# Optimization experiments

Measured on AMD Instinct MI355X. Metric: run time of the kernel, lower is better.

The kernel has to match this reference:

```python
import jax, jax.numpy as jnp
import numpy as np

N = 32768          # nodes
E = 131072         # edges
H = 4              # heads
RNA = 128          # rna_feature_dim
PROT = 32          # prot_feature_dim
F0 = 64            # num_features_per_layer[0] == [1]
CIN = F0 + PROT    # cross-path feature dim (96)
LRELU = 0.2


def _param(key, shape):
    return jax.random.normal(key, shape, dtype=jnp.float32) * 0.1


def setup_inputs() -> dict:
    key = jax.random.key(0)
    ks = jax.random.split(key, 20)
    return {
        "rna_data": jax.random.normal(ks[0], (N, RNA), dtype=jnp.float32),
        "prot_data": jax.random.normal(ks[1], (N, PROT), dtype=jnp.float32),
        "edge_index": jax.random.randint(ks[2], (2, E), 0, N, dtype=jnp.int32),
        "W_gat_proj": _param(ks[3], (RNA, F0)),
        "b_gat_proj": _param(ks[4], (F0,)),
        "W_gat_reproj": _param(ks[5], (F0, RNA)),
        "b_gat_reproj": _param(ks[6], (RNA,)),
        "Wg": _param(ks[7], (F0, H * F0)),
        "ag_src": _param(ks[8], (H, F0)),
        "ag_trg": _param(ks[9], (H, F0)),
        "bg": _param(ks[10], (F0,)),
        "W_cross_proj": _param(ks[11], (RNA + PROT, CIN)),
        "b_cross_proj": _param(ks[12], (CIN,)),
        "W_cross_reproj": _param(ks[13], (CIN, RNA + PROT)),
        "b_cross_reproj": _param(ks[14], (RNA + PROT,)),
        "Wc": _param(ks[15], (CIN, H * CIN)),
        "ac_src": _param(ks[16], (H, CIN)),
        "ac_trg": _param(ks[17], (H, CIN)),
        "bc": _param(ks[18], (CIN,)),
    }


def gat_layer(x, W, a_src, a_trg, bias, edge_index, softmax_on_src):
    """GATLayer with concat=False, activation=None, skip connection (in==out dim),
    dropout in eval mode. CrossAttnLayer groups the edge-softmax by src instead of trg."""
    n, f = x.shape
    src, trg = edge_index[0], edge_index[1]
    proj = (x @ W).reshape(n, H, f)                               # [N,H,F] lift targets
    s_src = jnp.einsum('nhf,hf->nh', proj, a_src)                 # [N,H]
    s_trg = jnp.einsum('nhf,hf->nh', proj, a_trg)                 # [N,H]
    scores = jax.nn.leaky_relu(s_src[src] + s_trg[trg], LRELU)    # [E,H] per-edge scores
    grp = src if softmax_on_src else trg
    ex = jnp.exp(scores - scores.max())                           # global-max shift (as in source)
    denom = jax.ops.segment_sum(ex, grp, num_segments=n)          # [N,H]
    attn = ex / (denom[grp] + 1e-16)                              # neighborhood-aware softmax [E,H]
    weighted = proj[src] * attn[:, :, None]                       # [E,H,F]
    out = jax.ops.segment_sum(weighted, trg, num_segments=n)      # scatter-add aggregate [N,H,F]
    out = out + x[:, None, :]                                     # direct skip (out_dim == in_dim)
    out = out.mean(axis=1) + bias                                 # concat=False -> head mean, + bias
    return out                                                    # activation=None (last layer)


def reference(rna_data, prot_data, edge_index,
              W_gat_proj, b_gat_proj, W_gat_reproj, b_gat_reproj,
              Wg, ag_src, ag_trg, bg,
              W_cross_proj, b_cross_proj, W_cross_reproj, b_cross_reproj,
              Wc, ac_src, ac_trg, bc):
    concat = jnp.concatenate([rna_data, prot_data], axis=1)       # [N, RNA+PROT]
    rna_p = rna_data @ W_gat_proj + b_gat_proj                    # [N, F0]
    cross_p = concat @ W_cross_proj + b_cross_proj                # [N, CIN]
    gat_out = gat_layer(rna_p, Wg, ag_src, ag_trg, bg, edge_index, False)    # [N, F0]
    cross_out = gat_layer(cross_p, Wc, ac_src, ac_trg, bc, edge_index, True)  # [N, CIN]
    # CrossAttnLayer's trailing view(-1, num_heads, num_out_features)
    cross_out = cross_out.reshape(-1, H, CIN)                     # [N/H, H, CIN]
    gat_final = gat_out @ W_gat_reproj + b_gat_reproj             # [N, RNA]
    cross_final = cross_out @ W_cross_reproj + b_cross_reproj     # [N/H, H, RNA+PROT]
    return gat_final, cross_final
```

## Files before the change

kernel.cpp:

```cpp
#include <hip/hip_runtime.h>
#include <hip/hip_bf16.h>

#define NN 32768
#define NE 131072
#define HH 4

constexpr float kLrelu = 0.2f;

using bf16x8 = __attribute__((ext_vector_type(8))) __bf16;
using f32x4  = __attribute__((ext_vector_type(4))) float;

__device__ inline short f2b(float f) {
    __hip_bfloat16 h = __float2bfloat16(f);
    return __builtin_bit_cast(short, h);
}
__device__ inline float b2f(short s) {
    __hip_bfloat16 h = __builtin_bit_cast(__hip_bfloat16, s);
    return __bfloat162float(h);
}
__device__ inline float blo(int u) {
    return __builtin_bit_cast(float, (int)(u << 16));
}
__device__ inline float bhi(int u) {
    return __builtin_bit_cast(float, (int)(u & 0xffff0000));
}
__device__ inline float lrexp(float x) {
    return __expf(x > 0.f ? x : kLrelu * x);
}

template<int K, int LDA, int OUTN, int BM, int BN, bool BF16OUT>
__global__ __launch_bounds__(256) void mfma_gemm(
    const short* __restrict__ A, const short* __restrict__ Wt,
    const float* __restrict__ bias,
    float* __restrict__ Cf, short* __restrict__ Cb)
{
    constexpr int KP    = K + 8;
    constexpr int WM    = BM / 32;
    constexpr int WN    = 4 / WM;
    constexpr int WBN   = BN / WN;
    constexpr int CF    = WBN / 16;
    constexpr int CPR   = K / 8;
    constexpr int TOT   = (BM + BN) * KP;
    constexpr int SLICE = TOT / 4;

    __shared__ short lds[TOT];
    short* As = lds;
    short* Bs = lds + BM * KP;

    const int tid  = threadIdx.x;
    const int wave = tid >> 6;
    const int lane = tid & 63;
    const int lr   = lane & 15;
    const int kb   = lane >> 4;
    const int wm   = wave % WM;
    const int wn   = wave / WM;
    const int row0 = blockIdx.x * BM;
    const int col0 = blockIdx.y * BN;

    #pragma unroll
    for (int g = tid; g < BM * CPR; g += 256) {
        int r = g / CPR, c = g - r * CPR;
        bf16x8 v = *(const bf16x8*)(A + (size_t)(row0 + r) * LDA + c * 8);
        *(bf16x8*)(As + r * KP + c * 8) = v;
    }
    #pragma unroll
    for (int g = tid; g < BN * CPR; g += 256) {
        int r = g / CPR, c = g - r * CPR;
        bf16x8 v = *(const bf16x8*)(Wt + (size_t)(col0 + r) * K + c * 8);
        *(bf16x8*)(Bs + r * KP + c * 8) = v;
    }
    __syncthreads();

    f32x4 acc[2][CF] = {};
    #pragma unroll
    for (int k0 = 0; k0 < K; k0 += 32) {
        bf16x8 af0 = *(const bf16x8*)(As + (wm * 32 + lr     ) * KP + k0 + kb * 8);
        bf16x8 af1 = *(const bf16x8*)(As + (wm * 32 + lr + 16) * KP + k0 + kb * 8);
        #pragma unroll
        for (int cf = 0; cf < CF; ++cf) {
            bf16x8 bv = *(const bf16x8*)(Bs + (wn * WBN + cf * 16 + lr) * KP + k0 + kb * 8);
            acc[0][cf] = __builtin_amdgcn_mfma_f32_16x16x32_bf16(af0, bv, acc[0][cf], 0, 0, 0);
            acc[1][cf] = __builtin_amdgcn_mfma_f32_16x16x32_bf16(af1, bv, acc[1][cf], 0, 0, 0);
        }
    }

    #pragma unroll
    for (int mf = 0; mf < 2; ++mf) {
        __syncthreads();
        if constexpr (BF16OUT) {
            constexpr int LEP = WBN + 8;
            short* ep = lds + wave * SLICE;
            #pragma unroll
            for (int cf = 0; cf < CF; ++cf) {
                const int c  = cf * 16 + lr;
                const float bv = bias ? bias[col0 + wn * WBN + c] : 0.0f;
                #pragma unroll
                for (int j = 0; j < 4; ++j)
                    ep[(kb * 4 + j) * LEP + c] = f2b(acc[mf][cf][j] + bv);
            }
            __syncthreads();
            constexpr int CROW = WBN / 8;
            for (int g = lane; g < 16 * CROW; g += 64) {
                int r = g / CROW, cc = g - r * CROW;
                bf16x8 v = *(const bf16x8*)(ep + r * LEP + cc * 8);
                *(bf16x8*)(Cb + (size_t)(row0 + wm * 32 + mf * 16 + r) * OUTN
                              + col0 + wn * WBN + cc * 8) = v;
            }
        } else {
            constexpr int LEPF = WBN + 4;
            float* epf = (float*)(lds + wave * SLICE);
            #pragma unroll
            for (int cf = 0; cf < CF; ++cf) {
                const int c  = cf * 16 + lr;
                const float bv = bias ? bias[col0 + wn * WBN + c] : 0.0f;
                #pragma unroll
                for (int j = 0; j < 4; ++j)
                    epf[(kb * 4 + j) * LEPF + c] = acc[mf][cf][j] + bv;
            }
            __syncthreads();
            constexpr int CROWF = WBN / 4;
            for (int g = lane; g < 16 * CROWF; g += 64) {
                int r = g / CROWF, cc = g - r * CROWF;
                float4 v = *(const float4*)(epf + r * LEPF + cc * 4);
                *(float4*)(Cf + (size_t)(row0 + wm * 32 + mf * 16 + r) * OUTN
                              + col0 + wn * WBN + cc * 4) = v;
            }
        }
    }
}

template<int F>
__device__ inline void score_one(
    const short* __restrict__ proj_b,
    const float* __restrict__ a_src, const float* __restrict__ a_trg,
    float* __restrict__ ssrc, float* __restrict__ strg, int t)
{
    int n = t >> 2, h = t & 3;
    const int4* p = (const int4*)(proj_b + (size_t)n * (4 * F) + h * F);
    const float* as = a_src + h * F;
    const float* at = a_trg + h * F;
    float ss = 0.f, st = 0.f;
    #pragma unroll
    for (int c = 0; c < F / 8; ++c) {
        int4 v = p[c];
        int u[4] = { v.x, v.y, v.z, v.w };
        #pragma unroll
        for (int q = 0; q < 4; ++q) {
            float x0 = blo(u[q]), x1 = bhi(u[q]);
            ss += x0 * as[c * 8 + 2 * q] + x1 * as[c * 8 + 2 * q + 1];
            st += x0 * at[c * 8 + 2 * q] + x1 * at[c * 8 + 2 * q + 1];
        }
    }
    ssrc[t] = ss;
    strg[t] = st;
}

__global__ __launch_bounds__(256) void scores_both(
    const short* __restrict__ projG,
    const float* __restrict__ agsG, const float* __restrict__ agtG,
    float* __restrict__ ssrcG, float* __restrict__ strgG,
    const short* __restrict__ projC,
    const float* __restrict__ acsC, const float* __restrict__ actC,
    float* __restrict__ ssrcC, float* __restrict__ strgC)
{
    int t = blockIdx.x * 256 + threadIdx.x;
    if (t < NN * HH) score_one<64>(projG, agsG, agtG, ssrcG, strgG, t);
    else             score_one<96>(projC, acsC, actC, ssrcC, strgC, t - NN * HH);
}

__global__ __launch_bounds__(256) void prep_kernel(
    const float* __restrict__ rna, const float* __restrict__ prot,
    short* __restrict__ cb,
    const float* W0, const float* W1, const float* W2,
    const float* W3, const float* W4, const float* W5,
    short* T0, short* T1, short* T2, short* T3, short* T4, short* T5,
    int4* __restrict__ zero_p)
{
    const int bid = blockIdx.x;
    if (bid < 5120) {
        int t = bid * 256 + threadIdx.x;
        int n = t / 40, j = (t - n * 40) * 4;
        float4 v = (j < 128) ? *(const float4*)(rna  + (size_t)n * 128 + j)
                             : *(const float4*)(prot + (size_t)n * 32 + (j - 128));
        short4 o = { f2b(v.x), f2b(v.y), f2b(v.z), f2b(v.w) };
        *(short4*)(cb + (size_t)n * 160 + j) = o;
    } else if (bid < 5984) {
        int idx = bid - 5120;
        int wsel = idx / 144, sub = idx - wsel * 144;
        int K, N; const float* W; short* T;
        switch (wsel) {
            case 0: K = 128; N =  64; W = W0; T = T0; break;
            case 1: K =  64; N = 256; W = W1; T = T1; break;
            case 2: K =  64; N = 128; W = W2; T = T2; break;
            case 3: K = 160; N =  96; W = W3; T = T3; break;
            case 4: K =  96; N = 384; W = W4; T = T4; break;
            default:K =  96; N = 160; W = W5; T = T5; break;
        }
        int t = sub * 256 + threadIdx.x;
        if (t >= K * N) return;
        int n = t / K, k = t - n * K;
        T[t] = f2b(W[(size_t)k * N + n]);
    } else {
        zero_p[(bid - 5984) * 256 + threadIdx.x] = make_int4(0, 0, 0, 0);
    }
}

__global__ __launch_bounds__(256) void hist_dual(const int* __restrict__ ei,
                                                 int* __restrict__ deg_t,
                                                 int* __restrict__ deg_s)
{
    int e = blockIdx.x * 256 + threadIdx.x;
    if (e >= NE) return;
    atomicAdd(&deg_s[ei[e]], 1);
    atomicAdd(&deg_t[ei[NE + e]], 1);
}

__global__ __launch_bounds__(1024) void scan_dual(
    const int* __restrict__ deg_t, int* __restrict__ rowptr_t, int* __restrict__ cursor_t,
    const int* __restrict__ deg_s, int* __restrict__ rowptr_s, int* __restrict__ cursor_s)
{
    const int* deg    = blockIdx.x ? deg_s    : deg_t;
    int*       rowptr = blockIdx.x ? rowptr_s : rowptr_t;
    int*       cursor = blockIdx.x ? cursor_s : cursor_t;
    __shared__ int sums[1024];
    const int t = threadIdx.x;
    const int base = t * 32;
    int local[32];
    int s = 0;
    #pragma unroll
    for (int i = 0; i < 32; ++i) { local[i] = s; s += deg[base + i]; }
    sums[t] = s;
    __syncthreads();
    for (int off = 1; off < 1024; off <<= 1) {
        int v = (t >= off) ? sums[t - off] : 0;
        __syncthreads();
        sums[t] += v;
        __syncthreads();
    }
    const int prev = (t == 0) ? 0 : sums[t - 1];
    #pragma unroll
    for (int i = 0; i < 32; ++i) {
        rowptr[base + i] = prev + local[i];
        cursor[base + i] = prev + local[i];
    }
    if (t == 1023) rowptr[NN] = prev + s;
}

__global__ __launch_bounds__(256) void scatter_dual(
    const int* __restrict__ ei,
    int* __restrict__ cursor_t, int* __restrict__ csr_srcT,
    int* __restrict__ cursor_s, int* __restrict__ csr_trgS)
{
    int e = blockIdx.x * 256 + threadIdx.x;
    if (e >= NE) return;
    int s = ei[e], t = ei[NE + e];
    int st = atomicAdd(&cursor_t[t], 1);
    csr_srcT[st] = s;
    int ss = atomicAdd(&cursor_s[s], 1);
    csr_trgS[ss] = t;
}

__global__ __launch_bounds__(256) void den_src_kernel(
    const int* __restrict__ rowptr_s, const int* __restrict__ csr_trgS,
    const float* __restrict__ ssrc, const float* __restrict__ strg,
    float* __restrict__ recip)
{
    int n = blockIdx.x * 256 + threadIdx.x;
    if (n >= NN) return;
    const int beg = rowptr_s[n], end = rowptr_s[n + 1];
    const float4 sv = *(const float4*)(ssrc + 4 * (size_t)n);
    float d0 = 0.f, d1 = 0.f, d2 = 0.f, d3 = 0.f;
    for (int sl = beg; sl < end; ++sl) {
        const int t = csr_trgS[sl];
        const float4 tv = *(const float4*)(strg + 4 * (size_t)t);
        d0 += lrexp(sv.x + tv.x); d1 += lrexp(sv.y + tv.y);
        d2 += lrexp(sv.z + tv.z); d3 += lrexp(sv.w + tv.w);
    }
    *(float4*)(recip + 4 * (size_t)n) =
        make_float4(1.f / (d0 + 1e-16f), 1.f / (d1 + 1e-16f),
                    1.f / (d2 + 1e-16f), 1.f / (d3 + 1e-16f));
}

template<int F, int NPB, bool GROUP_SRC>
__global__ __launch_bounds__((F / 2) * NPB) void aggregate_fused(
    const int* __restrict__ rowptr_t, const int* __restrict__ csr_srcT,
    const float* __restrict__ ssrc, const float* __restrict__ strg,
    const float* __restrict__ recip,
    const short* __restrict__ proj_b,
    const short* __restrict__ x_pb, const float* __restrict__ bias,
    short* __restrict__ aggb)
{
    const int f2   = threadIdx.x * 2;
    const int node = blockIdx.x * NPB + threadIdx.y;
    const int beg  = rowptr_t[node], end = rowptr_t[node + 1];
    const float4 stv = *(const float4*)(strg + 4 * (size_t)node);

    float a0 = 0.f, a1 = 0.f;
    float h0l = 0.f, h1l = 0.f, h2l = 0.f, h3l = 0.f;
    float h0h = 0.f, h1h = 0.f, h2h = 0.f, h3h = 0.f;
    float d0 = 0.f, d1 = 0.f, d2 = 0.f, d3 = 0.f;

    #pragma unroll 4
    for (int sl = beg; sl < end; ++sl) {
        const int s = csr_srcT[sl];
        const float4 sv = *(const float4*)(ssrc + 4 * (size_t)s);
        float e0 = lrexp(sv.x + stv.x);
        float e1 = lrexp(sv.y + stv.y);
        float e2 = lrexp(sv.z + stv.z);
        float e3 = lrexp(sv.w + stv.w);
        const short* p = proj_b + (size_t)s * (4 * F) + f2;
        const int u0 = *(const int*)(p);
        const int u1 = *(const int*)(p + F);
        const int u2 = *(const int*)(p + 2 * F);
        const int u3 = *(const int*)(p + 3 * F);
        if constexpr (GROUP_SRC) {
            const float4 rc = *(const float4*)(recip + 4 * (size_t)s);
            e0 *= rc.x; e1 *= rc.y; e2 *= rc.z; e3 *= rc.w;
            a0 += e0 * blo(u0) + e1 * blo(u1) + e2 * blo(u2) + e3 * blo(u3);
            a1 += e0 * bhi(u0) + e1 * bhi(u1) + e2 * bhi(u2) + e3 * bhi(u3);
        } else {
            d0 += e0; d1 += e1; d2 += e2; d3 += e3;
            h0l += e0 * blo(u0); h0h += e0 * bhi(u0);
            h1l += e1 * blo(u1); h1h += e1 * bhi(u1);
            h2l += e2 * blo(u2); h2h += e2 * bhi(u2);
            h3l += e3 * blo(u3); h3h += e3 * bhi(u3);
        }
    }
    if constexpr (!GROUP_SRC) {
        const float r0 = 1.f / (d0 + 1e-16f), r1 = 1.f / (d1 + 1e-16f);
        const float r2 = 1.f / (d2 + 1e-16f), r3 = 1.f / (d3 + 1e-16f);
        a0 = h0l * r0 + h1l * r1 + h2l * r2 + h3l * r3;
        a1 = h0h * r0 + h1h * r1 + h2h * r2 + h3h * r3;
    }
    const int o = node * F + f2;
    const int ux = *(const int*)(x_pb + o);
    const float v0 = a0 * 0.25f + blo(ux) + bias[f2];
    const float v1 = a1 * 0.25f + bhi(ux) + bias[f2 + 1];
    *(int*)(aggb + o) = (f2b(v0) & 0xffff) | ((int)f2b(v1) << 16);
}

extern "C" void kernel_launch(void* const* d_in, const int* in_sizes, int n_in,
                              void* d_out, int out_size, void* d_ws, size_t ws_size,
                              hipStream_t stream)
{
    const float* rna   = (const float*)d_in[0];
    const float* prot  = (const float*)d_in[1];
    const int*   ei    = (const int*)  d_in[2];
    const float* Wgp   = (const float*)d_in[3];
    const float* bgp   = (const float*)d_in[4];
    const float* Wgr   = (const float*)d_in[5];
    const float* bgr   = (const float*)d_in[6];
    const float* Wg    = (const float*)d_in[7];
    const float* ags   = (const float*)d_in[8];
    const float* agt   = (const float*)d_in[9];
    const float* bg    = (const float*)d_in[10];
    const float* Wcp   = (const float*)d_in[11];
    const float* bcp   = (const float*)d_in[12];
    const float* Wcr   = (const float*)d_in[13];
    const float* bcr   = (const float*)d_in[14];
    const float* Wc    = (const float*)d_in[15];
    const float* acs   = (const float*)d_in[16];
    const float* act   = (const float*)d_in[17];
    const float* bc    = (const float*)d_in[18];

    float* out_gat   = (float*)d_out;
    float* out_cross = out_gat + (size_t)NN * 128;

    float* ssrcG  = (float*)d_ws;
    float* strgG  = ssrcG + (size_t)NN * 4;
    float* ssrcC  = strgG + (size_t)NN * 4;
    float* strgC  = ssrcC + (size_t)NN * 4;
    float* recip  = strgC + (size_t)NN * 4;
    short* projG  = (short*)(recip + (size_t)NN * 4);
    short* projC  = projG + (size_t)NN * 256;
    short* cb     = projC + (size_t)NN * 384;
    short* x_pG   = cb    + (size_t)NN * 160;
    short* x_pC   = x_pG  + (size_t)NN * 64;
    short* aggG   = x_pC  + (size_t)NN * 96;
    short* aggC   = aggG  + (size_t)NN * 64;
    short* wt_gp  = aggC  + (size_t)NN * 96;
    short* wt_g   = wt_gp + 128 * 64;
    short* wt_gr  = wt_g  + 64 * 256;
    short* wt_cp  = wt_gr + 64 * 128;
    short* wt_c   = wt_cp + 160 * 96;
    short* wt_cr  = wt_c  + 96 * 384;
    int*   deg_t  = (int*)(wt_cr + 96 * 160);
    int*   deg_s  = deg_t  + NN;
    int*   cursor_t = deg_s  + NN;
    int*   cursor_s = cursor_t + NN;
    int*   rowptr_t = cursor_s + NN;
    int*   rowptr_s = rowptr_t + NN + 1;
    int*   csr_srcT = rowptr_s + NN + 1;
    int*   csr_trgS = csr_srcT + NE;

    prep_kernel<<<6048, 256, 0, stream>>>(rna, prot, cb,
                                          Wgp, Wg, Wgr, Wcp, Wc, Wcr,
                                          wt_gp, wt_g, wt_gr, wt_cp, wt_c, wt_cr,
                                          (int4*)deg_t);
    hist_dual<<<NE / 256, 256, 0, stream>>>(ei, deg_t, deg_s);
    scan_dual<<<2, 1024, 0, stream>>>(deg_t, rowptr_t, cursor_t, deg_s, rowptr_s, cursor_s);
    scatter_dual<<<NE / 256, 256, 0, stream>>>(ei, cursor_t, csr_srcT, cursor_s, csr_trgS);

    mfma_gemm<128, 160,  64, 32,  64, true ><<<dim3(1024, 1), 256, 0, stream>>>(cb,   wt_gp, bgp, nullptr, x_pG);
    mfma_gemm<160, 160,  96, 64,  96, true ><<<dim3( 512, 1), 256, 0, stream>>>(cb,   wt_cp, bcp, nullptr, x_pC);
    mfma_gemm< 64,  64, 256, 64, 128, true ><<<dim3( 512, 2), 256, 0, stream>>>(x_pG, wt_g,  nullptr, nullptr, projG);
    mfma_gemm< 96,  96, 384, 64, 128, true ><<<dim3( 512, 3), 256, 0, stream>>>(x_pC, wt_c,  nullptr, nullptr, projC);

    scores_both<<<(2 * NN * HH) / 256, 256, 0, stream>>>(
        projG, ags, agt, ssrcG, strgG, projC, acs, act, ssrcC, strgC);
    den_src_kernel<<<NN / 256, 256, 0, stream>>>(rowptr_s, csr_trgS, ssrcC, strgC, recip);

    aggregate_fused<64, 8, false><<<NN / 8, dim3(32, 8), 0, stream>>>(
        rowptr_t, csr_srcT, ssrcG, strgG, nullptr, projG, x_pG, bg, aggG);
    aggregate_fused<96, 8, true><<<NN / 8, dim3(48, 8), 0, stream>>>(
        rowptr_t, csr_srcT, ssrcC, strgC, recip, projC, x_pC, bc, aggC);

    mfma_gemm< 64,  64, 128, 64,  64, false><<<dim3(512, 2), 256, 0, stream>>>(aggG, wt_gr, bgr, out_gat, nullptr);
    mfma_gemm< 96,  96, 160, 64, 160, false><<<dim3(512, 1), 256, 0, stream>>>(aggC, wt_cr, bcr, out_cross, nullptr);
}
```

Measured before the change: 182.0 us.

## Merge paired GEMM and aggregation launches into combined dual-grid kernels

```diff
diff --git a/kernel.cpp b/kernel.cpp
--- a/kernel.cpp
+++ b/kernel.cpp
@@ -29,10 +29,11 @@
 }
 
 template<int K, int LDA, int OUTN, int BM, int BN, bool BF16OUT>
-__global__ __launch_bounds__(256) void mfma_gemm(
+__device__ __forceinline__ void gemm_dev(
     const short* __restrict__ A, const short* __restrict__ Wt,
     const float* __restrict__ bias,
-    float* __restrict__ Cf, short* __restrict__ Cb)
+    float* __restrict__ Cf, short* __restrict__ Cb,
+    short* lds, int bx, int by)
 {
     constexpr int KP    = K + 8;
     constexpr int WM    = BM / 32;
@@ -43,7 +44,6 @@
     constexpr int TOT   = (BM + BN) * KP;
     constexpr int SLICE = TOT / 4;
 
-    __shared__ short lds[TOT];
     short* As = lds;
     short* Bs = lds + BM * KP;
 
@@ -54,8 +54,8 @@
     const int kb   = lane >> 4;
     const int wm   = wave % WM;
     const int wn   = wave / WM;
-    const int row0 = blockIdx.x * BM;
-    const int col0 = blockIdx.y * BN;
+    const int row0 = bx * BM;
+    const int col0 = by * BN;
 
     #pragma unroll
     for (int g = tid; g < BM * CPR; g += 256) {
@@ -129,6 +129,29 @@
     }
 }
 
+template<int K1, int LDA1, int OUTN1, int BM1, int BN1, bool BO1,
+         int K2, int LDA2, int OUTN2, int BM2, int BN2, bool BO2>
+__global__ __launch_bounds__(256) void dual_gemm(
+    const short* A1, const short* Wt1, const float* b1, float* Cf1, short* Cb1,
+    int nbx1, int nby1,
+    const short* A2, const short* Wt2, const float* b2, float* Cf2, short* Cb2,
+    int nbx2, int nby2)
+{
+    constexpr int TOT1 = (BM1 + BN1) * (K1 + 8);
+    constexpr int TOT2 = (BM2 + BN2) * (K2 + 8);
+    constexpr int TOT  = TOT1 > TOT2 ? TOT1 : TOT2;
+    __shared__ short lds[TOT];
+    if (blockIdx.z == 0) {
+        if ((int)blockIdx.x < nbx1 && (int)blockIdx.y < nby1)
+            gemm_dev<K1, LDA1, OUTN1, BM1, BN1, BO1>(A1, Wt1, b1, Cf1, Cb1, lds,
+                                                     blockIdx.x, blockIdx.y);
+    } else {
+        if ((int)blockIdx.x < nbx2 && (int)blockIdx.y < nby2)
+            gemm_dev<K2, LDA2, OUTN2, BM2, BN2, BO2>(A2, Wt2, b2, Cf2, Cb2, lds,
+                                                     blockIdx.x, blockIdx.y);
+    }
+}
+
 template<int F>
 __device__ inline void score_one(
     const short* __restrict__ proj_b,
@@ -281,8 +304,9 @@
                     1.f / (d2 + 1e-16f), 1.f / (d3 + 1e-16f));
 }
 
-template<int F, int NPB, bool GROUP_SRC>
-__global__ __launch_bounds__((F / 2) * NPB) void aggregate_fused(
+template<int F, bool GROUP_SRC>
+__device__ __forceinline__ void agg_body(
+    int f2, int node,
     const int* __restrict__ rowptr_t, const int* __restrict__ csr_srcT,
     const float* __restrict__ ssrc, const float* __restrict__ strg,
     const float* __restrict__ recip,
@@ -290,9 +314,7 @@
     const short* __restrict__ x_pb, const float* __restrict__ bias,
     short* __restrict__ aggb)
 {
-    const int f2   = threadIdx.x * 2;
-    const int node = blockIdx.x * NPB + threadIdx.y;
-    const int beg  = rowptr_t[node], end = rowptr_t[node + 1];
+    const int beg = rowptr_t[node], end = rowptr_t[node + 1];
     const float4 stv = *(const float4*)(strg + 4 * (size_t)node);
 
     float a0 = 0.f, a1 = 0.f;
@@ -300,7 +322,7 @@
     float h0h = 0.f, h1h = 0.f, h2h = 0.f, h3h = 0.f;
     float d0 = 0.f, d1 = 0.f, d2 = 0.f, d3 = 0.f;
 
-    #pragma unroll 4
+    #pragma unroll 2
     for (int sl = beg; sl < end; ++sl) {
         const int s = csr_srcT[sl];
         const float4 sv = *(const float4*)(ssrc + 4 * (size_t)s);
@@ -337,6 +359,34 @@
     const float v0 = a0 * 0.25f + blo(ux) + bias[f2];
     const float v1 = a1 * 0.25f + bhi(ux) + bias[f2 + 1];
     *(int*)(aggb + o) = (f2b(v0) & 0xffff) | ((int)f2b(v1) << 16);
+}
+
+#define GAT_BLKS 2731
+__global__ __launch_bounds__(384) void aggregate_mega(
+    const int* __restrict__ rowptr_t, const int* __restrict__ csr_srcT,
+    const float* __restrict__ ssrcG, const float* __restrict__ strgG,
+    const float* __restrict__ ssrcC, const float* __restrict__ strgC,
+    const float* __restrict__ recip,
+    const short* __restrict__ projG, const short* __restrict__ projC,
+    const short* __restrict__ xG, const short* __restrict__ xC,
+    const float* __restrict__ biasG, const float* __restrict__ biasC,
+    short* __restrict__ aggG, short* __restrict__ aggC)
+{
+    const int bid = blockIdx.x;
+    const int tid = threadIdx.x;
+    if (bid < GAT_BLKS) {
+        const int node = bid * 12 + tid / 32;
+        const int f2   = (tid & 31) * 2;
+        if (node >= NN) return;
+        agg_body<64, false>(f2, node, rowptr_t, csr_srcT, ssrcG, strgG,
+                            nullptr, projG, xG, biasG, aggG);
+    } else {
+        const int b    = bid - GAT_BLKS;
+        const int node = b * 8 + tid / 48;
+        const int f2   = (tid % 48) * 2;
+        agg_body<96, true>(f2, node, rowptr_t, csr_srcT, ssrcC, strgC,
+                           recip, projC, xC, biasC, aggC);
+    }
 }
 
 extern "C" void kernel_launch(void* const* d_in, const int* in_sizes, int n_in,
@@ -401,20 +451,26 @@
     scan_dual<<<2, 1024, 0, stream>>>(deg_t, rowptr_t, cursor_t, deg_s, rowptr_s, cursor_s);
     scatter_dual<<<NE / 256, 256, 0, stream>>>(ei, cursor_t, csr_srcT, cursor_s, csr_trgS);
 
-    mfma_gemm<128, 160,  64, 32,  64, true ><<<dim3(1024, 1), 256, 0, stream>>>(cb,   wt_gp, bgp, nullptr, x_pG);
-    mfma_gemm<160, 160,  96, 64,  96, true ><<<dim3( 512, 1), 256, 0, stream>>>(cb,   wt_cp, bcp, nullptr, x_pC);
-    mfma_gemm< 64,  64, 256, 64, 128, true ><<<dim3( 512, 2), 256, 0, stream>>>(x_pG, wt_g,  nullptr, nullptr, projG);
-    mfma_gemm< 96,  96, 384, 64, 128, true ><<<dim3( 512, 3), 256, 0, stream>>>(x_pC, wt_c,  nullptr, nullptr, projC);
+    dual_gemm<128, 160,  64, 32,  64, true,
+              160, 160,  96, 64,  96, true><<<dim3(1024, 1, 2), 256, 0, stream>>>(
+        cb, wt_gp, bgp, nullptr, x_pG, 1024, 1,
+        cb, wt_cp, bcp, nullptr, x_pC,  512, 1);
+
+    dual_gemm< 64,  64, 256, 64, 128, true,
+               96,  96, 384, 64, 128, true><<<dim3(512, 3, 2), 256, 0, stream>>>(
+        x_pG, wt_g, nullptr, nullptr, projG, 512, 2,
+        x_pC, wt_c, nullptr, nullptr, projC, 512, 3);
 
     scores_both<<<(2 * NN * HH) / 256, 256, 0, stream>>>(
         projG, ags, agt, ssrcG, strgG, projC, acs, act, ssrcC, strgC);
     den_src_kernel<<<NN / 256, 256, 0, stream>>>(rowptr_s, csr_trgS, ssrcC, strgC, recip);
 
-    aggregate_fused<64, 8, false><<<NN / 8, dim3(32, 8), 0, stream>>>(
-        rowptr_t, csr_srcT, ssrcG, strgG, nullptr, projG, x_pG, bg, aggG);
-    aggregate_fused<96, 8, true><<<NN / 8, dim3(48, 8), 0, stream>>>(
-        rowptr_t, csr_srcT, ssrcC, strgC, recip, projC, x_pC, bc, aggC);
-
-    mfma_gemm< 64,  64, 128, 64,  64, false><<<dim3(512, 2), 256, 0, stream>>>(aggG, wt_gr, bgr, out_gat, nullptr);
-    mfma_gemm< 96,  96, 160, 64, 160, false><<<dim3(512, 1), 256, 0, stream>>>(aggC, wt_cr, bcr, out_cross, nullptr);
-}
+    aggregate_mega<<<GAT_BLKS + NN / 8, 384, 0, stream>>>(
+        rowptr_t, csr_srcT, ssrcG, strgG, ssrcC, strgC, recip,
+        projG, projC, x_pG, x_pC, bg, bc, aggG, aggC);
+
+    dual_gemm< 64,  64, 128, 64,  64, false,
+               96,  96, 160, 64, 160, false><<<dim3(512, 2, 2), 256, 0, stream>>>(
+        aggG, wt_gr, bgr, out_gat,   nullptr, 512, 2,
+        aggC, wt_cr, bcr, out_cross, nullptr, 512, 1);
+}
```

Measured after the change: 167.2 us (median of 3 runs). 1.09x faster.
